# Optimization experiments

Measured on AMD Instinct MI355X. Metric: run time of the kernel, lower is better.

Reference implementation:

```python
import jax, jax.numpy as jnp
import numpy as np
import math

JULIA_ITERS = 64
ESCAPE_RADIUS = 2.0


def _julia_escape_times(seq_len, c_real, c_imag):
    # Positions mapped to the real segment [-2, 2]; iterate z <- z^2 + c,
    # record (first iteration index where |z| > R) / ITERS, else 1.0.
    x = jnp.linspace(-2.0, 2.0, seq_len)
    zr0 = x
    zi0 = jnp.zeros_like(x)
    escaped0 = jnp.zeros(seq_len, dtype=bool)
    et0 = jnp.ones(seq_len, dtype=x.dtype)
    r2 = ESCAPE_RADIUS * ESCAPE_RADIUS

    def step(carry, it):
        zr, zi, escaped, et = carry
        nzr = zr * zr - zi * zi + c_real
        nzi = 2.0 * zr * zi + c_imag
        # torch breaks out of the loop once escaped -> freeze z afterwards
        zr = jnp.where(escaped, zr, nzr)
        zi = jnp.where(escaped, zi, nzi)
        mag2 = zr * zr + zi * zi
        newly = jnp.logical_and(~escaped, mag2 > r2)
        et = jnp.where(newly, it.astype(et.dtype) / JULIA_ITERS, et)
        escaped = jnp.logical_or(escaped, newly)
        return (zr, zi, escaped, et), None

    (_, _, _, et), _ = jax.lax.scan(step, (zr0, zi0, escaped0, et0), jnp.arange(JULIA_ITERS))
    return et


def setup_inputs() -> dict:
    key = jax.random.key(0)
    kq, kk, kv = jax.random.split(key, 3)
    B, S, D = 4, 8192, 64
    return {
        "query": jax.random.normal(kq, (B, S, D), dtype=jnp.float32),
        "key": jax.random.normal(kk, (B, S, D), dtype=jnp.float32),
        "value": jax.random.normal(kv, (B, S, D), dtype=jnp.float32),
        "julia_c_real": jnp.float32(-0.7),
        "julia_c_imag": jnp.float32(0.27),
        "escape_scale": jnp.float32(1.0),
    }


def reference(query, key, value, julia_c_real, julia_c_imag, escape_scale):
    B, S, D = key.shape
    et = _julia_escape_times(S, julia_c_real, julia_c_imag)            # [S]
    julia_weights = jnp.exp(et * escape_scale)                          # [S]
    bias = jnp.log(julia_weights + 1e-8)                                # [S]
    scores = jnp.einsum("bqd,bkd->bqk", query, key) / math.sqrt(D)     # [B,S,S]
    scores = scores + bias[None, None, :]
    attn = jax.nn.softmax(scores, axis=-1)
    out = jnp.einsum("bqk,bkd->bqd", attn, value)                       # [B,S,D]
    return out  # squeeze(1) is a no-op for S > 1
```

## Files before the change

kernel.cpp:

```cpp
#include <hip/hip_runtime.h>
#include <math.h>

#define S_LEN 8192
#define DHEAD 64
#define NBATCH 4
#define BK 32
#define KIT 64

typedef unsigned short u16;
typedef unsigned int u32;
typedef __attribute__((ext_vector_type(8))) _Float16 half8;
typedef __attribute__((ext_vector_type(2))) __fp16 fp16x2;
typedef __attribute__((ext_vector_type(4))) float f32x4;

union HU8 { int4 i4; half8 h8; u32 w[4]; };
union H2U { fp16x2 h2; u32 w; };
union HU  { _Float16 h; u16 u; };

#if __has_builtin(__builtin_amdgcn_exp2f)
#define EXP2(x) __builtin_amdgcn_exp2f(x)
#else
#define EXP2(x) exp2f(x)
#endif

__device__ __forceinline__ u16 f2h(float f) {
    HU x; x.h = (_Float16)f; return x.u;
}
__device__ __forceinline__ u32 packh2(float a, float b) {
    H2U x; x.h2 = __builtin_amdgcn_cvt_pkrtz(a, b); return x.w;
}

__global__ void prep_kernel(const float* __restrict__ K, const float* __restrict__ V,
                            const float* crp, const float* cip, const float* scp,
                            u16* __restrict__ blob, float* __restrict__ bias2) {
    int bid = blockIdx.x, tid = threadIdx.x;
    if (bid < 1024) {
        int b = bid >> 8, t = bid & 255;
        __shared__ float Kt[32 * 64];
        __shared__ float Vt[32 * 65];
        int row = tid >> 3, c8 = (tid & 7) * 8;
        const float* ks = K + ((size_t)(b * S_LEN + t * 32 + row)) * 64 + c8;
        const float* vs = V + ((size_t)(b * S_LEN + t * 32 + row)) * 64 + c8;
        float4 ka = *(const float4*)ks, kb4 = *(const float4*)(ks + 4);
        float4 va = *(const float4*)vs, vb4 = *(const float4*)(vs + 4);
        *(float4*)&Kt[row * 64 + c8] = ka;
        *(float4*)&Kt[row * 64 + c8 + 4] = kb4;
        float* vr = &Vt[row * 65 + c8];
        vr[0] = va.x; vr[1] = va.y; vr[2] = va.z; vr[3] = va.w;
        vr[4] = vb4.x; vr[5] = vb4.y; vr[6] = vb4.z; vr[7] = vb4.w;
        __syncthreads();

        int j = tid >> 6, lane = tid & 63, low = lane & 15, h = lane >> 4;
        u16* tb = blob + ((size_t)(b * 256 + t)) * 4096;
        {
            int kt = j >> 1, ds = j & 1;
            int krow = 8 * (low >> 2) + 4 * kt + (low & 3);
            const float* src = &Kt[krow * 64 + ds * 32 + h * 8];
            u32 wds[4];
#pragma unroll
            for (int i = 0; i < 4; ++i)
                wds[i] = (u32)f2h(src[2 * i]) | ((u32)f2h(src[2 * i + 1]) << 16);
            *(int4*)(tb + j * 512 + lane * 8) = make_int4(wds[0], wds[1], wds[2], wds[3]);
        }
        {
            int col = j * 16 + low;
            u32 wds[4];
#pragma unroll
            for (int i = 0; i < 4; ++i) {
                float a = Vt[(h * 8 + 2 * i) * 65 + col];
                float c = Vt[(h * 8 + 2 * i + 1) * 65 + col];
                wds[i] = (u32)f2h(a) | ((u32)f2h(c) << 16);
            }
            *(int4*)(tb + 2048 + j * 512 + lane * 8) = make_int4(wds[0], wds[1], wds[2], wds[3]);
        }
    } else {
#pragma clang fp contract(off)
        int i = (bid - 1024) * 256 + tid;
        double cr = (double)crp[0], ci = (double)cip[0], sc = (double)scp[0];
        double step = 4.0 / (double)(S_LEN - 1);
        double x = (i == S_LEN - 1) ? 2.0 : (-2.0 + step * (double)i);
        double zr = x, zi = 0.0, et = 1.0;
        bool esc = false;
        for (int it = 0; it < 64; ++it) {
            double nzr = zr * zr - zi * zi + cr;
            double nzi = 2.0 * zr * zi + ci;
            if (!esc) { zr = nzr; zi = nzi; }
            double m2 = zr * zr + zi * zi;
            if (!esc && m2 > 4.0) { et = (double)it / 64.0; esc = true; }
        }
        double bias = log(exp(et * sc) + 1e-8);
        bias2[i] = (float)(bias * 1.4426950408889634 - 20.0);
    }
}

__global__ __launch_bounds__(256, 2)
void flash_kernel(const float* __restrict__ Q, const u16* __restrict__ blob,
                  const float* __restrict__ bias2, float* __restrict__ Out) {
    __shared__ __align__(16) char smem[17664];

    const int tid = threadIdx.x;
    const int l = tid & 63, low = l & 15, h = l >> 4;
    const int kq = __builtin_amdgcn_readfirstlane(tid >> 6);

    const int bid = blockIdx.x;
    const int batch = bid & 3;
    const int qtile = bid >> 2;
    const int q0 = qtile * 64;

    const float qscale = 0.18033688011112042f;
    half8 qfrag[4][2];
#pragma unroll
    for (int qf = 0; qf < 4; ++qf) {
        const float* qrow = Q + ((size_t)(batch * S_LEN + q0 + qf * 16 + low)) * DHEAD + h * 8;
#pragma unroll
        for (int ds = 0; ds < 2; ++ds) {
            f32x4 a = *(const f32x4*)(qrow + ds * 32);
            f32x4 b = *(const f32x4*)(qrow + ds * 32 + 4);
            HU8 u;
            u.w[0] = packh2(a[0] * qscale, a[1] * qscale);
            u.w[1] = packh2(a[2] * qscale, a[3] * qscale);
            u.w[2] = packh2(b[0] * qscale, b[1] * qscale);
            u.w[3] = packh2(b[2] * qscale, b[3] * qscale);
            qfrag[qf][ds] = u.h8;
        }
    }

    const u16* kvb = blob + ((size_t)(batch * 256 + kq * 64)) * 4096;
    const int loff = l * 8;
    const float* bbase = bias2 + kq * 2048;

    f32x4 o[4][4];
#pragma unroll
    for (int qf = 0; qf < 4; ++qf)
#pragma unroll
        for (int dt = 0; dt < 4; ++dt) o[qf][dt] = (f32x4){0, 0, 0, 0};
    float lsum[4] = {0.f, 0.f, 0.f, 0.f};

    HU8 kf[2][4];
    f32x4 bvv[2][2];
#pragma unroll
    for (int j = 0; j < 4; ++j) kf[0][j].i4 = *(const int4*)(kvb + j * 512 + loff);
    bvv[0][0] = *(const f32x4*)(bbase + h * 8);
    bvv[0][1] = *(const f32x4*)(bbase + h * 8 + 4);

#pragma unroll 2
    for (int ki = 0; ki < KIT; ++ki) {
        const int c = ki & 1;
        const u16* tb = kvb + ki * 4096;

        HU8 vf[4];
#pragma unroll
        for (int j = 0; j < 4; ++j) vf[j].i4 = *(const int4*)(tb + 2048 + j * 512 + loff);

        const u16* tn = tb + 4096;
#pragma unroll
        for (int j = 0; j < 4; ++j) kf[c ^ 1][j].i4 = *(const int4*)(tn + j * 512 + loff);
        const float* bpn = bbase + (ki + 1) * 32 + h * 8;
        bvv[c ^ 1][0] = *(const f32x4*)bpn;
        bvv[c ^ 1][1] = *(const f32x4*)(bpn + 4);

        HU8 pf[4];
#pragma unroll
        for (int kt = 0; kt < 2; ++kt) {
            const f32x4 binit = kt ? bvv[c][1] : bvv[c][0];
            f32x4 st[4];
#pragma unroll
            for (int qf = 0; qf < 4; ++qf) {
                f32x4 a = __builtin_amdgcn_mfma_f32_16x16x32_f16(kf[c][kt * 2].h8, qfrag[qf][0], binit, 0, 0, 0);
                a = __builtin_amdgcn_mfma_f32_16x16x32_f16(kf[c][kt * 2 + 1].h8, qfrag[qf][1], a, 0, 0, 0);
                st[qf] = a;
            }
#pragma unroll
            for (int qf = 0; qf < 4; ++qf) {
                float p0 = EXP2(st[qf][0]), p1 = EXP2(st[qf][1]);
                float p2 = EXP2(st[qf][2]), p3 = EXP2(st[qf][3]);
                lsum[qf] += (p0 + p1) + (p2 + p3);
                pf[qf].w[kt * 2]     = packh2(p0, p1);
                pf[qf].w[kt * 2 + 1] = packh2(p2, p3);
            }
        }

#pragma unroll
        for (int dt = 0; dt < 4; ++dt)
#pragma unroll
            for (int qf = 0; qf < 4; ++qf)
                o[qf][dt] = __builtin_amdgcn_mfma_f32_16x16x32_f16(vf[dt].h8, pf[qf].h8, o[qf][dt], 0, 0, 0);
    }

#pragma unroll
    for (int qf = 0; qf < 4; ++qf) {
        lsum[qf] += __shfl_xor(lsum[qf], 16, 64);
        lsum[qf] += __shfl_xor(lsum[qf], 32, 64);
    }

    float* MO = (float*)smem;
    float* ML = (float*)(smem + 17408);
#pragma unroll 1
    for (int src = 1; src < 4; ++src) {
        __syncthreads();
        if (kq == src) {
#pragma unroll
            for (int qf = 0; qf < 4; ++qf) {
                const int row = qf * 16 + low;
#pragma unroll
                for (int dt = 0; dt < 4; ++dt)
                    *(f32x4*)&MO[row * 68 + dt * 16 + h * 4] = o[qf][dt];
                if (h == 0) ML[row] = lsum[qf];
            }
        }
        __syncthreads();
        if (kq == 0) {
#pragma unroll
            for (int qf = 0; qf < 4; ++qf) {
                const int row = qf * 16 + low;
#pragma unroll
                for (int dt = 0; dt < 4; ++dt) {
                    f32x4 a = *(const f32x4*)&MO[row * 68 + dt * 16 + h * 4];
#pragma unroll
                    for (int jj = 0; jj < 4; ++jj) o[qf][dt][jj] += a[jj];
                }
                lsum[qf] += ML[row];
            }
        }
    }

    if (kq == 0) {
#pragma unroll
        for (int qf = 0; qf < 4; ++qf) {
            const float inv = 1.f / lsum[qf];
            float* orow = Out + ((size_t)(batch * S_LEN + q0 + qf * 16 + low)) * DHEAD;
#pragma unroll
            for (int dt = 0; dt < 4; ++dt) {
                f32x4 r;
#pragma unroll
                for (int jj = 0; jj < 4; ++jj) r[jj] = o[qf][dt][jj] * inv;
                *(f32x4*)(orow + dt * 16 + h * 4) = r;
            }
        }
    }
}

extern "C" void kernel_launch(void* const* d_in, const int* in_sizes, int n_in,
                              void* d_out, int out_size, void* d_ws, size_t ws_size,
                              hipStream_t stream) {
    const float* Q  = (const float*)d_in[0];
    const float* K  = (const float*)d_in[1];
    const float* V  = (const float*)d_in[2];
    const float* cr = (const float*)d_in[3];
    const float* ci = (const float*)d_in[4];
    const float* sc = (const float*)d_in[5];
    float* out = (float*)d_out;

    char* ws = (char*)d_ws;
    float* bias2 = (float*)ws;
    u16*   blob  = (u16*)(ws + 32768);

    prep_kernel<<<dim3(1056), dim3(256), 0, stream>>>(K, V, cr, ci, sc, blob, bias2);
    flash_kernel<<<dim3(512), dim3(256), 0, stream>>>(Q, blob, bias2, out);
}
```

Before: 151.5 us.

## Software-pipeline attention loop so PV MFMAs overlap next tile's QK and softmax

Restructures the key-tile loop into a skewed software pipeline. Each iteration issues the QK^T MFMAs for tile i, then the PV MFMAs for tile i-1 using the previously computed probabilities, then exp/softmax for tile i. The point is to keep the matrix units busy while exp2 and packing run and to hide V load latency by double-buffering V fragments. This costs more live registers (two V buffers plus scores), which may cut occupancy or cause spills. The loop is manually unrolled by two with a prologue and epilogue.

```diff
diff --git a/kernel.cpp b/kernel.cpp
--- a/kernel.cpp
+++ b/kernel.cpp
@@ -138,54 +138,83 @@
 
     HU8 kf[2][4];
     f32x4 bvv[2][2];
+    HU8 vf[2][4];
+    HU8 pf[4];
+
+    auto QK = [&](const HU8 (&kfc)[4], const f32x4 (&bvc)[2], f32x4 (&st)[2][4]) {
+#pragma unroll
+        for (int kt = 0; kt < 2; ++kt) {
+            const f32x4 binit = bvc[kt];
+#pragma unroll
+            for (int qf = 0; qf < 4; ++qf) {
+                f32x4 a = __builtin_amdgcn_mfma_f32_16x16x32_f16(kfc[kt * 2].h8, qfrag[qf][0], binit, 0, 0, 0);
+                a = __builtin_amdgcn_mfma_f32_16x16x32_f16(kfc[kt * 2 + 1].h8, qfrag[qf][1], a, 0, 0, 0);
+                st[kt][qf] = a;
+            }
+        }
+    };
+    auto SM = [&](const f32x4 (&st)[2][4]) {
+#pragma unroll
+        for (int kt = 0; kt < 2; ++kt)
+#pragma unroll
+            for (int qf = 0; qf < 4; ++qf) {
+                float p0 = EXP2(st[kt][qf][0]), p1 = EXP2(st[kt][qf][1]);
+                float p2 = EXP2(st[kt][qf][2]), p3 = EXP2(st[kt][qf][3]);
+                lsum[qf] += (p0 + p1) + (p2 + p3);
+                pf[qf].w[kt * 2]     = packh2(p0, p1);
+                pf[qf].w[kt * 2 + 1] = packh2(p2, p3);
+            }
+    };
+    auto PV = [&](const HU8 (&vfc)[4]) {
+#pragma unroll
+        for (int dt = 0; dt < 4; ++dt)
+#pragma unroll
+            for (int qf = 0; qf < 4; ++qf)
+                o[qf][dt] = __builtin_amdgcn_mfma_f32_16x16x32_f16(vfc[dt].h8, pf[qf].h8, o[qf][dt], 0, 0, 0);
+    };
+
 #pragma unroll
     for (int j = 0; j < 4; ++j) kf[0][j].i4 = *(const int4*)(kvb + j * 512 + loff);
     bvv[0][0] = *(const f32x4*)(bbase + h * 8);
     bvv[0][1] = *(const f32x4*)(bbase + h * 8 + 4);
-
-#pragma unroll 2
-    for (int ki = 0; ki < KIT; ++ki) {
-        const int c = ki & 1;
-        const u16* tb = kvb + ki * 4096;
-
-        HU8 vf[4];
-#pragma unroll
-        for (int j = 0; j < 4; ++j) vf[j].i4 = *(const int4*)(tb + 2048 + j * 512 + loff);
-
-        const u16* tn = tb + 4096;
-#pragma unroll
-        for (int j = 0; j < 4; ++j) kf[c ^ 1][j].i4 = *(const int4*)(tn + j * 512 + loff);
-        const float* bpn = bbase + (ki + 1) * 32 + h * 8;
-        bvv[c ^ 1][0] = *(const f32x4*)bpn;
-        bvv[c ^ 1][1] = *(const f32x4*)(bpn + 4);
-
-        HU8 pf[4];
-#pragma unroll
-        for (int kt = 0; kt < 2; ++kt) {
-            const f32x4 binit = kt ? bvv[c][1] : bvv[c][0];
-            f32x4 st[4];
-#pragma unroll
-            for (int qf = 0; qf < 4; ++qf) {
-                f32x4 a = __builtin_amdgcn_mfma_f32_16x16x32_f16(kf[c][kt * 2].h8, qfrag[qf][0], binit, 0, 0, 0);
-                a = __builtin_amdgcn_mfma_f32_16x16x32_f16(kf[c][kt * 2 + 1].h8, qfrag[qf][1], a, 0, 0, 0);
-                st[qf] = a;
-            }
-#pragma unroll
-            for (int qf = 0; qf < 4; ++qf) {
-                float p0 = EXP2(st[qf][0]), p1 = EXP2(st[qf][1]);
-                float p2 = EXP2(st[qf][2]), p3 = EXP2(st[qf][3]);
-                lsum[qf] += (p0 + p1) + (p2 + p3);
-                pf[qf].w[kt * 2]     = packh2(p0, p1);
-                pf[qf].w[kt * 2 + 1] = packh2(p2, p3);
-            }
-        }
-
-#pragma unroll
-        for (int dt = 0; dt < 4; ++dt)
-#pragma unroll
-            for (int qf = 0; qf < 4; ++qf)
-                o[qf][dt] = __builtin_amdgcn_mfma_f32_16x16x32_f16(vf[dt].h8, pf[qf].h8, o[qf][dt], 0, 0, 0);
-    }
+#pragma unroll
+    for (int j = 0; j < 4; ++j) vf[0][j].i4 = *(const int4*)(kvb + 2048 + j * 512 + loff);
+#pragma unroll
+    for (int j = 0; j < 4; ++j) kf[1][j].i4 = *(const int4*)(kvb + 4096 + j * 512 + loff);
+    bvv[1][0] = *(const f32x4*)(bbase + 32 + h * 8);
+    bvv[1][1] = *(const f32x4*)(bbase + 32 + h * 8 + 4);
+    {
+        f32x4 st0[2][4];
+        QK(kf[0], bvv[0], st0);
+        SM(st0);
+    }
+
+#define BODY(KI, C)                                                              \
+    {                                                                            \
+        const u16* tb_ = kvb + (size_t)(KI) * 4096;                              \
+        _Pragma("unroll")                                                        \
+        for (int j = 0; j < 4; ++j)                                              \
+            vf[C][j].i4 = *(const int4*)(tb_ + 2048 + j * 512 + loff);           \
+        _Pragma("unroll")                                                        \
+        for (int j = 0; j < 4; ++j)                                              \
+            kf[(C) ^ 1][j].i4 = *(const int4*)(tb_ + 4096 + j * 512 + loff);     \
+        const float* bpn_ = bbase + ((KI) + 1) * 32 + h * 8;                     \
+        bvv[(C) ^ 1][0] = *(const f32x4*)bpn_;                                   \
+        bvv[(C) ^ 1][1] = *(const f32x4*)(bpn_ + 4);                             \
+        f32x4 st_[2][4];                                                         \
+        QK(kf[C], bvv[C], st_);                                                  \
+        PV(vf[(C) ^ 1]);                                                         \
+        SM(st_);                                                                 \
+    }
+
+#pragma unroll 1
+    for (int kp = 1; kp < KIT - 1; kp += 2) {
+        BODY(kp, 1)
+        BODY(kp + 1, 0)
+    }
+    BODY(KIT - 1, 1)
+    PV(vf[1]);
+#undef BODY
 
 #pragma unroll
     for (int qf = 0; qf < 4; ++qf) {
```

New measurement: 150.8 us. No clear change (-0.5%).

## Split KV sequence across six waves per block with tree reduction

Applied to the files above, without the earlier changes.

Each block now runs 384 threads (six waves) instead of four. The waves split the 256 KV tiles 43/43/43/43/42/42, which raises the number of waves resident per CU to better hide memory latency. The cross-wave merge becomes a two-level tree through larger shared memory. The K/V register double buffer is replaced by single-buffered loads issued after the QK and PV MFMAs, and the workspace offset is padded for the bias over-read. The risks are register pressure under the waves_per_eu(3) cap, less prefetch distance, and more LDS and sync traffic in the reduction.

```diff
diff --git a/kernel.cpp b/kernel.cpp
--- a/kernel.cpp
+++ b/kernel.cpp
@@ -5,7 +5,6 @@
 #define DHEAD 64
 #define NBATCH 4
 #define BK 32
-#define KIT 64
 
 typedef unsigned short u16;
 typedef unsigned int u32;
@@ -93,14 +92,15 @@
     }
 }
 
-__global__ __launch_bounds__(256, 2)
+__global__ __launch_bounds__(384)
+__attribute__((amdgpu_waves_per_eu(3)))
 void flash_kernel(const float* __restrict__ Q, const u16* __restrict__ blob,
                   const float* __restrict__ bias2, float* __restrict__ Out) {
-    __shared__ __align__(16) char smem[17664];
+    __shared__ __align__(16) char smem[52992];
 
     const int tid = threadIdx.x;
     const int l = tid & 63, low = l & 15, h = l >> 4;
-    const int kq = __builtin_amdgcn_readfirstlane(tid >> 6);
+    const int ks = __builtin_amdgcn_readfirstlane(tid >> 6);
 
     const int bid = blockIdx.x;
     const int batch = bid & 3;
@@ -125,9 +125,12 @@
         }
     }
 
-    const u16* kvb = blob + ((size_t)(batch * 256 + kq * 64)) * 4096;
+    const int t0  = (ks < 4) ? ks * 43 : 172 + (ks - 4) * 42;
+    const int kit = (ks < 4) ? 43 : 42;
+
+    const u16* kvb = blob + ((size_t)(batch * 256 + t0)) * 4096;
     const int loff = l * 8;
-    const float* bbase = bias2 + kq * 2048;
+    const float* bbase = bias2 + t0 * 32;
 
     f32x4 o[4][4];
 #pragma unroll
@@ -136,55 +139,58 @@
         for (int dt = 0; dt < 4; ++dt) o[qf][dt] = (f32x4){0, 0, 0, 0};
     float lsum[4] = {0.f, 0.f, 0.f, 0.f};
 
-    HU8 kf[2][4];
-    f32x4 bvv[2][2];
-#pragma unroll
-    for (int j = 0; j < 4; ++j) kf[0][j].i4 = *(const int4*)(kvb + j * 512 + loff);
-    bvv[0][0] = *(const f32x4*)(bbase + h * 8);
-    bvv[0][1] = *(const f32x4*)(bbase + h * 8 + 4);
-
-#pragma unroll 2
-    for (int ki = 0; ki < KIT; ++ki) {
-        const int c = ki & 1;
-        const u16* tb = kvb + ki * 4096;
-
-        HU8 vf[4];
-#pragma unroll
-        for (int j = 0; j < 4; ++j) vf[j].i4 = *(const int4*)(tb + 2048 + j * 512 + loff);
-
-        const u16* tn = tb + 4096;
-#pragma unroll
-        for (int j = 0; j < 4; ++j) kf[c ^ 1][j].i4 = *(const int4*)(tn + j * 512 + loff);
+    HU8 kf[4];
+    f32x4 bvv[2];
+    HU8 vf[4];
+
+#pragma unroll
+    for (int j = 0; j < 4; ++j) kf[j].i4 = *(const int4*)(kvb + j * 512 + loff);
+    bvv[0] = *(const f32x4*)(bbase + h * 8);
+    bvv[1] = *(const f32x4*)(bbase + h * 8 + 4);
+#pragma unroll
+    for (int j = 0; j < 4; ++j) vf[j].i4 = *(const int4*)(kvb + 2048 + j * 512 + loff);
+
+#pragma unroll 1
+    for (int ki = 0; ki < kit; ++ki) {
+        f32x4 st[2][4];
+#pragma unroll
+        for (int kt = 0; kt < 2; ++kt) {
+            const f32x4 binit = kt ? bvv[1] : bvv[0];
+#pragma unroll
+            for (int qf = 0; qf < 4; ++qf) {
+                f32x4 a = __builtin_amdgcn_mfma_f32_16x16x32_f16(kf[kt * 2].h8, qfrag[qf][0], binit, 0, 0, 0);
+                a = __builtin_amdgcn_mfma_f32_16x16x32_f16(kf[kt * 2 + 1].h8, qfrag[qf][1], a, 0, 0, 0);
+                st[kt][qf] = a;
+            }
+        }
+
+        const u16* tn = kvb + ((size_t)ki + 1) * 4096;
+#pragma unroll
+        for (int j = 0; j < 4; ++j) kf[j].i4 = *(const int4*)(tn + j * 512 + loff);
         const float* bpn = bbase + (ki + 1) * 32 + h * 8;
-        bvv[c ^ 1][0] = *(const f32x4*)bpn;
-        bvv[c ^ 1][1] = *(const f32x4*)(bpn + 4);
+        bvv[0] = *(const f32x4*)bpn;
+        bvv[1] = *(const f32x4*)(bpn + 4);
 
         HU8 pf[4];
 #pragma unroll
-        for (int kt = 0; kt < 2; ++kt) {
-            const f32x4 binit = kt ? bvv[c][1] : bvv[c][0];
-            f32x4 st[4];
+        for (int kt = 0; kt < 2; ++kt)
 #pragma unroll
             for (int qf = 0; qf < 4; ++qf) {
-                f32x4 a = __builtin_amdgcn_mfma_f32_16x16x32_f16(kf[c][kt * 2].h8, qfrag[qf][0], binit, 0, 0, 0);
-                a = __builtin_amdgcn_mfma_f32_16x16x32_f16(kf[c][kt * 2 + 1].h8, qfrag[qf][1], a, 0, 0, 0);
-                st[qf] = a;
-            }
-#pragma unroll
-            for (int qf = 0; qf < 4; ++qf) {
-                float p0 = EXP2(st[qf][0]), p1 = EXP2(st[qf][1]);
-                float p2 = EXP2(st[qf][2]), p3 = EXP2(st[qf][3]);
+                float p0 = EXP2(st[kt][qf][0]), p1 = EXP2(st[kt][qf][1]);
+                float p2 = EXP2(st[kt][qf][2]), p3 = EXP2(st[kt][qf][3]);
                 lsum[qf] += (p0 + p1) + (p2 + p3);
                 pf[qf].w[kt * 2]     = packh2(p0, p1);
                 pf[qf].w[kt * 2 + 1] = packh2(p2, p3);
             }
-        }
 
 #pragma unroll
         for (int dt = 0; dt < 4; ++dt)
 #pragma unroll
             for (int qf = 0; qf < 4; ++qf)
                 o[qf][dt] = __builtin_amdgcn_mfma_f32_16x16x32_f16(vf[dt].h8, pf[qf].h8, o[qf][dt], 0, 0, 0);
+
+#pragma unroll
+        for (int j = 0; j < 4; ++j) vf[j].i4 = *(const int4*)(tn + 2048 + j * 512 + loff);
     }
 
 #pragma unroll
@@ -193,38 +199,45 @@
         lsum[qf] += __shfl_xor(lsum[qf], 32, 64);
     }
 
-    float* MO = (float*)smem;
-    float* ML = (float*)(smem + 17408);
-#pragma unroll 1
-    for (int src = 1; src < 4; ++src) {
-        __syncthreads();
-        if (kq == src) {
-#pragma unroll
-            for (int qf = 0; qf < 4; ++qf) {
-                const int row = qf * 16 + low;
-#pragma unroll
-                for (int dt = 0; dt < 4; ++dt)
-                    *(f32x4*)&MO[row * 68 + dt * 16 + h * 4] = o[qf][dt];
-                if (h == 0) ML[row] = lsum[qf];
-            }
-        }
-        __syncthreads();
-        if (kq == 0) {
-#pragma unroll
-            for (int qf = 0; qf < 4; ++qf) {
-                const int row = qf * 16 + low;
-#pragma unroll
-                for (int dt = 0; dt < 4; ++dt) {
-                    f32x4 a = *(const f32x4*)&MO[row * 68 + dt * 16 + h * 4];
-#pragma unroll
-                    for (int jj = 0; jj < 4; ++jj) o[qf][dt][jj] += a[jj];
-                }
-                lsum[qf] += ML[row];
-            }
-        }
-    }
-
-    if (kq == 0) {
+    auto wpart = [&](int slot) {
+        float* MO = (float*)(smem + slot * 17664);
+        float* ML = (float*)(smem + slot * 17664 + 17408);
+#pragma unroll
+        for (int qf = 0; qf < 4; ++qf) {
+            const int row = qf * 16 + low;
+#pragma unroll
+            for (int dt = 0; dt < 4; ++dt)
+                *(f32x4*)&MO[row * 68 + dt * 16 + h * 4] = o[qf][dt];
+            if (h == 0) ML[row] = lsum[qf];
+        }
+    };
+    auto apart = [&](int slot) {
+        float* MO = (float*)(smem + slot * 17664);
+        float* ML = (float*)(smem + slot * 17664 + 17408);
+#pragma unroll
+        for (int qf = 0; qf < 4; ++qf) {
+            const int row = qf * 16 + low;
+#pragma unroll
+            for (int dt = 0; dt < 4; ++dt) {
+                f32x4 a = *(const f32x4*)&MO[row * 68 + dt * 16 + h * 4];
+#pragma unroll
+                for (int jj = 0; jj < 4; ++jj) o[qf][dt][jj] += a[jj];
+            }
+            lsum[qf] += ML[row];
+        }
+    };
+
+    __syncthreads();
+    if (ks & 1) wpart(ks >> 1);
+    __syncthreads();
+    if (!(ks & 1)) apart(ks >> 1);
+    __syncthreads();
+    if (ks == 2) wpart(0);
+    if (ks == 4) wpart(1);
+    __syncthreads();
+    if (ks == 0) { apart(0); apart(1); }
+
+    if (ks == 0) {
 #pragma unroll
         for (int qf = 0; qf < 4; ++qf) {
             const float inv = 1.f / lsum[qf];
@@ -253,8 +266,8 @@
 
     char* ws = (char*)d_ws;
     float* bias2 = (float*)ws;
-    u16*   blob  = (u16*)(ws + 32768);
+    u16*   blob  = (u16*)(ws + 33024);
 
     prep_kernel<<<dim3(1056), dim3(256), 0, stream>>>(K, V, cr, ci, sc, blob, bias2);
-    flash_kernel<<<dim3(512), dim3(256), 0, stream>>>(Q, blob, bias2, out);
-}
+    flash_kernel<<<dim3(512), dim3(384), 0, stream>>>(Q, blob, bias2, out);
+}
```

Result: slower. 247.1 us (+63.0%).

## Software-pipeline QK^T MFMA one tile ahead of exp and PV in flash loop

Applied to the files above, without the earlier changes.

Restructures the attention inner loop so the score MFMAs for tile k+1 are issued before the exp/pack and PV MFMAs of tile k, using ping-pong score registers (stA/stB) and a prologue and epilogue. The aim is to overlap the transcendental exp work with matrix-core work and hide K/V load latency. The blob offset is shifted slightly, likely to make room for bias reads one tile past the end. It raises register pressure from the two score buffers, which could cut occupancy.

```diff
diff --git a/kernel.cpp b/kernel.cpp
--- a/kernel.cpp
+++ b/kernel.cpp
@@ -136,56 +136,100 @@
         for (int dt = 0; dt < 4; ++dt) o[qf][dt] = (f32x4){0, 0, 0, 0};
     float lsum[4] = {0.f, 0.f, 0.f, 0.f};
 
-    HU8 kf[2][4];
-    f32x4 bvv[2][2];
-#pragma unroll
-    for (int j = 0; j < 4; ++j) kf[0][j].i4 = *(const int4*)(kvb + j * 512 + loff);
-    bvv[0][0] = *(const f32x4*)(bbase + h * 8);
-    bvv[0][1] = *(const f32x4*)(bbase + h * 8 + 4);
-
-#pragma unroll 2
-    for (int ki = 0; ki < KIT; ++ki) {
-        const int c = ki & 1;
-        const u16* tb = kvb + ki * 4096;
-
-        HU8 vf[4];
-#pragma unroll
-        for (int j = 0; j < 4; ++j) vf[j].i4 = *(const int4*)(tb + 2048 + j * 512 + loff);
-
-        const u16* tn = tb + 4096;
-#pragma unroll
-        for (int j = 0; j < 4; ++j) kf[c ^ 1][j].i4 = *(const int4*)(tn + j * 512 + loff);
-        const float* bpn = bbase + (ki + 1) * 32 + h * 8;
-        bvv[c ^ 1][0] = *(const f32x4*)bpn;
-        bvv[c ^ 1][1] = *(const f32x4*)(bpn + 4);
-
-        HU8 pf[4];
-#pragma unroll
-        for (int kt = 0; kt < 2; ++kt) {
-            const f32x4 binit = kt ? bvv[c][1] : bvv[c][0];
-            f32x4 st[4];
-#pragma unroll
-            for (int qf = 0; qf < 4; ++qf) {
-                f32x4 a = __builtin_amdgcn_mfma_f32_16x16x32_f16(kf[c][kt * 2].h8, qfrag[qf][0], binit, 0, 0, 0);
-                a = __builtin_amdgcn_mfma_f32_16x16x32_f16(kf[c][kt * 2 + 1].h8, qfrag[qf][1], a, 0, 0, 0);
-                st[qf] = a;
-            }
-#pragma unroll
-            for (int qf = 0; qf < 4; ++qf) {
-                float p0 = EXP2(st[qf][0]), p1 = EXP2(st[qf][1]);
-                float p2 = EXP2(st[qf][2]), p3 = EXP2(st[qf][3]);
-                lsum[qf] += (p0 + p1) + (p2 + p3);
-                pf[qf].w[kt * 2]     = packh2(p0, p1);
-                pf[qf].w[kt * 2 + 1] = packh2(p2, p3);
-            }
-        }
-
-#pragma unroll
-        for (int dt = 0; dt < 4; ++dt)
-#pragma unroll
-            for (int qf = 0; qf < 4; ++qf)
-                o[qf][dt] = __builtin_amdgcn_mfma_f32_16x16x32_f16(vf[dt].h8, pf[qf].h8, o[qf][dt], 0, 0, 0);
-    }
+    HU8 kf[4];
+    f32x4 bvv[2];
+    HU8 vf[4];
+    HU8 pf[4];
+    f32x4 stA[2][4];
+    f32x4 stB[2][4];
+
+#pragma unroll
+    for (int j = 0; j < 4; ++j) kf[j].i4 = *(const int4*)(kvb + j * 512 + loff);
+    bvv[0] = *(const f32x4*)(bbase + h * 8);
+    bvv[1] = *(const f32x4*)(bbase + h * 8 + 4);
+#pragma unroll
+    for (int kt = 0; kt < 2; ++kt) {
+        const f32x4 binit = kt ? bvv[1] : bvv[0];
+#pragma unroll
+        for (int qf = 0; qf < 4; ++qf) {
+            f32x4 a = __builtin_amdgcn_mfma_f32_16x16x32_f16(kf[kt * 2].h8, qfrag[qf][0], binit, 0, 0, 0);
+            a = __builtin_amdgcn_mfma_f32_16x16x32_f16(kf[kt * 2 + 1].h8, qfrag[qf][1], a, 0, 0, 0);
+            stA[kt][qf] = a;
+        }
+    }
+#pragma unroll
+    for (int j = 0; j < 4; ++j) kf[j].i4 = *(const int4*)(kvb + 4096 + j * 512 + loff);
+    bvv[0] = *(const f32x4*)(bbase + 32 + h * 8);
+    bvv[1] = *(const f32x4*)(bbase + 32 + h * 8 + 4);
+#pragma unroll
+    for (int j = 0; j < 4; ++j) vf[j].i4 = *(const int4*)(kvb + 2048 + j * 512 + loff);
+
+#define BODY(KI, STC, STP)                                                       \
+    {                                                                            \
+        const u16* tb_ = kvb + (size_t)(KI) * 4096;                              \
+        const u16* tn_ = tb_ + 4096;                                             \
+        _Pragma("unroll")                                                        \
+        for (int kt = 0; kt < 2; ++kt) {                                         \
+            const f32x4 binit = kt ? bvv[1] : bvv[0];                            \
+            _Pragma("unroll")                                                    \
+            for (int qf = 0; qf < 4; ++qf) {                                     \
+                f32x4 a = __builtin_amdgcn_mfma_f32_16x16x32_f16(                \
+                    kf[kt * 2].h8, qfrag[qf][0], binit, 0, 0, 0);                \
+                a = __builtin_amdgcn_mfma_f32_16x16x32_f16(                      \
+                    kf[kt * 2 + 1].h8, qfrag[qf][1], a, 0, 0, 0);                \
+                STC[kt][qf] = a;                                                 \
+            }                                                                    \
+        }                                                                        \
+        _Pragma("unroll")                                                        \
+        for (int j = 0; j < 4; ++j)                                              \
+            kf[j].i4 = *(const int4*)(tn_ + j * 512 + loff);                     \
+        const float* bpn_ = bbase + ((KI) + 1) * 32 + h * 8;                     \
+        bvv[0] = *(const f32x4*)bpn_;                                            \
+        bvv[1] = *(const f32x4*)(bpn_ + 4);                                      \
+        _Pragma("unroll")                                                        \
+        for (int kt = 0; kt < 2; ++kt)                                           \
+            _Pragma("unroll")                                                    \
+            for (int qf = 0; qf < 4; ++qf) {                                     \
+                float p0 = EXP2(STP[kt][qf][0]), p1 = EXP2(STP[kt][qf][1]);      \
+                float p2 = EXP2(STP[kt][qf][2]), p3 = EXP2(STP[kt][qf][3]);      \
+                lsum[qf] += (p0 + p1) + (p2 + p3);                               \
+                pf[qf].w[kt * 2]     = packh2(p0, p1);                           \
+                pf[qf].w[kt * 2 + 1] = packh2(p2, p3);                           \
+            }                                                                    \
+        _Pragma("unroll")                                                        \
+        for (int dt = 0; dt < 4; ++dt)                                           \
+            _Pragma("unroll")                                                    \
+            for (int qf = 0; qf < 4; ++qf)                                       \
+                o[qf][dt] = __builtin_amdgcn_mfma_f32_16x16x32_f16(              \
+                    vf[dt].h8, pf[qf].h8, o[qf][dt], 0, 0, 0);                   \
+        _Pragma("unroll")                                                        \
+        for (int j = 0; j < 4; ++j)                                              \
+            vf[j].i4 = *(const int4*)(tb_ + 2048 + j * 512 + loff);              \
+    }
+
+#pragma unroll 1
+    for (int kp = 1; kp < KIT - 1; kp += 2) {
+        BODY(kp, stB, stA)
+        BODY(kp + 1, stA, stB)
+    }
+    BODY(KIT - 1, stB, stA)
+#undef BODY
+
+#pragma unroll
+    for (int kt = 0; kt < 2; ++kt)
+#pragma unroll
+        for (int qf = 0; qf < 4; ++qf) {
+            float p0 = EXP2(stB[kt][qf][0]), p1 = EXP2(stB[kt][qf][1]);
+            float p2 = EXP2(stB[kt][qf][2]), p3 = EXP2(stB[kt][qf][3]);
+            lsum[qf] += (p0 + p1) + (p2 + p3);
+            pf[qf].w[kt * 2]     = packh2(p0, p1);
+            pf[qf].w[kt * 2 + 1] = packh2(p2, p3);
+        }
+#pragma unroll
+    for (int dt = 0; dt < 4; ++dt)
+#pragma unroll
+        for (int qf = 0; qf < 4; ++qf)
+            o[qf][dt] = __builtin_amdgcn_mfma_f32_16x16x32_f16(vf[dt].h8, pf[qf].h8, o[qf][dt], 0, 0, 0);
 
 #pragma unroll
     for (int qf = 0; qf < 4; ++qf) {
@@ -253,7 +297,7 @@
 
     char* ws = (char*)d_ws;
     float* bias2 = (float*)ws;
-    u16*   blob  = (u16*)(ws + 32768);
+    u16*   blob  = (u16*)(ws + 33024);
 
     prep_kernel<<<dim3(1056), dim3(256), 0, stream>>>(K, V, cr, ci, sc, blob, bias2);
     flash_kernel<<<dim3(512), dim3(256), 0, stream>>>(Q, blob, bias2, out);
```

Result: faster. 147.1 us (-2.9%).
